# Performance work log

Hardware: AMD Instinct MI355X
Metric: run time of the kernel (lower is better)

The kernel has to match this reference:

```python
import jax, jax.numpy as jnp
import numpy as np

B = 64            # batch of graphs
E = 8978          # edge-simplices per graph (nodes of the Hodge-1 graph)
E2 = E // 2       # after Graclus pair-pooling
K = 4             # Laguerre polynomial order
DEG = 16          # avg degree of the (edge-)adjacency
SLOPE = 0.33      # LeakyReLU negative slope
EPS = 1e-5        # BatchNorm eps


def _make_edges(rng, b, n, deg):
    # block-diagonal batched edge list: each graph only connects within itself
    offs = np.repeat(np.arange(b, dtype=np.int64) * n, n * deg)
    dst = np.tile(np.repeat(np.arange(n, dtype=np.int64), deg), b) + offs
    src = rng.integers(0, n, size=b * n * deg) + offs
    return np.stack([src, dst]).astype(np.int32)


def setup_inputs() -> dict:
    rng = np.random.default_rng(0)
    ks = jax.random.split(jax.random.key(0), 12)
    N1 = B * E
    ei1 = _make_edges(rng, B, E, DEG)
    ei2 = _make_edges(rng, B, E2, DEG)
    return {
        "x_s": jax.random.normal(ks[0], (N1, 1), jnp.float32),
        "edge_index_s": jnp.asarray(ei1),
        "edge_weight_s": jax.random.uniform(ks[1], (ei1.shape[1],), jnp.float32) * (2.0 / DEG),
        "edge_index_s1": jnp.asarray(ei2),
        "edge_weight_s1": jax.random.uniform(ks[2], (ei2.shape[1],), jnp.float32) * (2.0 / DEG),
        "W0": jax.random.normal(ks[3], (K, 1, 32), jnp.float32) * 0.3,
        "b0": jnp.zeros((32,), jnp.float32),
        "g0": jnp.ones((32,), jnp.float32),
        "be0": jnp.zeros((32,), jnp.float32),
        "W1": jax.random.normal(ks[4], (K, 32, 32), jnp.float32) * 0.1,
        "b1": jnp.zeros((32,), jnp.float32),
        "g1": jnp.ones((32,), jnp.float32),
        "be1": jnp.zeros((32,), jnp.float32),
        "W2": jax.random.normal(ks[5], (K, 32, 1), jnp.float32) * 0.1,
        "b2": jnp.zeros((1,), jnp.float32),
        "g2": jnp.ones((1,), jnp.float32),
        "be2": jnp.zeros((1,), jnp.float32),
        "lin1_W": jax.random.normal(ks[6], (E2, 256), jnp.float32) * 0.02,
        "lin1_b": jnp.zeros((256,), jnp.float32),
        "bn1_g": jnp.ones((256,), jnp.float32),
        "bn1_b": jnp.zeros((256,), jnp.float32),
        "lin2_W": jax.random.normal(ks[7], (256, 128), jnp.float32) * 0.06,
        "lin2_b": jnp.zeros((128,), jnp.float32),
        "bn2_g": jnp.ones((128,), jnp.float32),
        "bn2_b": jnp.zeros((128,), jnp.float32),
        "lin3_W": jax.random.normal(ks[8], (128, 1), jnp.float32) * 0.09,
        "lin3_b": jnp.zeros((1,), jnp.float32),
    }


def _laguerre_layer(x, src, dst, ew, W, b, gamma, beta, n):
    """HodgeLaguerreConv (K-order Laguerre recurrence over sparse L) + BatchNorm + LeakyReLU."""
    def matvec(v):  # (L v)[i] = sum_j w_ij v[j]
        return jax.ops.segment_sum(ew[:, None] * v[src], dst, num_segments=n)
    Tp = x                      # L_0(L) x = x
    out = Tp @ W[0]
    Tc = x - matvec(x)          # L_1(L) x = x - L x
    out = out + Tc @ W[1]
    for k in range(1, K - 1):   # L_{k+1} = ((2k+1-L) L_k - k L_{k-1}) / (k+1)
        Tn = ((2 * k + 1) * Tc - matvec(Tc) - k * Tp) / (k + 1)
        out = out + Tn @ W[k + 1]
        Tp, Tc = Tc, Tn
    out = out + b
    out = gamma * (out - out.mean(0)) * jax.lax.rsqrt(out.var(0) + EPS) + beta
    return jnp.where(out > 0, out, SLOPE * out)


def _bn(h, g, b):
    return g * (h - h.mean(0)) * jax.lax.rsqrt(h.var(0) + EPS) + b


def reference(x_s, edge_index_s, edge_weight_s, edge_index_s1, edge_weight_s1,
              W0, b0, g0, be0, W1, b1, g1, be1, W2, b2, g2, be2,
              lin1_W, lin1_b, bn1_g, bn1_b, lin2_W, lin2_b, bn2_g, bn2_b,
              lin3_W, lin3_b):
    N1, N2 = B * E, B * E2
    x = _laguerre_layer(x_s, edge_index_s[0], edge_index_s[1], edge_weight_s,
                        W0, b0, g0, be0, N1)
    # Graclus pooling: merge matched node pairs by max over features
    x = x.reshape(B, E2, 2, x.shape[-1]).max(axis=2).reshape(N2, -1)
    x = _laguerre_layer(x, edge_index_s1[0], edge_index_s1[1], edge_weight_s1,
                        W1, b1, g1, be1, N2)
    x = _laguerre_layer(x, edge_index_s1[0], edge_index_s1[1], edge_weight_s1,
                        W2, b2, g2, be2, N2)
    x = x.reshape(B, E2)        # last conv has 1 channel
    h = jax.nn.relu(_bn(x @ lin1_W + lin1_b, bn1_g, bn1_b))
    h = jax.nn.relu(_bn(h @ lin2_W + lin2_b, bn2_g, bn2_b))
    return h @ lin3_W + lin3_b  # [B, num_classes=1]
```

## Files before the change

### kernel.cpp

```cpp
#include <hip/hip_runtime.h>
#include <cstdint>

#define SLOPE 0.33f

static constexpr int B_   = 64;
static constexpr int E1_  = 8978;
static constexpr int E2_  = 4489;
static constexpr int N1_  = B_ * E1_;
static constexpr int N2_  = B_ * E2_;
static constexpr int DEG_ = 16;
static constexpr int QTR_ = 2245;
static constexpr int QTR2_ = 1123;
static constexpr int MVGRID = (N2_ * 32) / 256;
static constexpr double EPS_ = 1e-5;

typedef unsigned short u16;
typedef unsigned int   u32;

__device__ __forceinline__ float lrelu(float v) { return v > 0.f ? v : SLOPE * v; }
__device__ __forceinline__ float dot4(float4 a, float4 b) {
  return a.x * b.x + a.y * b.y + a.z * b.z + a.w * b.w;
}
__device__ __forceinline__ void gacc(float4& acc, float wgt, const float4& gv) {
  acc.x += wgt * gv.x; acc.y += wgt * gv.y; acc.z += wgt * gv.z; acc.w += wgt * gv.w;
}

template<int NPG>
__global__ __launch_bounds__(256) void k_prep(const int* __restrict__ src, int nNodes,
    u16* __restrict__ out) {
  int node = blockIdx.x * 256 + threadIdx.x;
  if (node >= nNodes) return;
  int gbase = (node / NPG) * NPG;
  const int4* s4 = (const int4*)(src + (size_t)node * DEG_);
  int4 a = s4[0], b = s4[1], c = s4[2], d = s4[3];
  uint4 o0, o1;
  o0.x = (u32)(a.x - gbase) | ((u32)(a.y - gbase) << 16);
  o0.y = (u32)(a.z - gbase) | ((u32)(a.w - gbase) << 16);
  o0.z = (u32)(b.x - gbase) | ((u32)(b.y - gbase) << 16);
  o0.w = (u32)(b.z - gbase) | ((u32)(b.w - gbase) << 16);
  o1.x = (u32)(c.x - gbase) | ((u32)(c.y - gbase) << 16);
  o1.y = (u32)(c.z - gbase) | ((u32)(c.w - gbase) << 16);
  o1.z = (u32)(d.x - gbase) | ((u32)(d.y - gbase) << 16);
  o1.w = (u32)(d.z - gbase) | ((u32)(d.w - gbase) << 16);
  uint4* op = (uint4*)(out + (size_t)node * DEG_);
  op[0] = o0; op[1] = o1;
}

#define GATHER1(dst, sv, si_, w4_)                                              \
  {                                                                             \
    uint4 A_ = si_[0], Bq_ = si_[1];                                            \
    float4 w_;                                                                  \
    w_ = w4_[0];                                                                \
    dst += w_.x * sv[A_.x & 0xFFFFu] + w_.y * sv[A_.x >> 16]                    \
         + w_.z * sv[A_.y & 0xFFFFu] + w_.w * sv[A_.y >> 16];                   \
    w_ = w4_[1];                                                                \
    dst += w_.x * sv[A_.z & 0xFFFFu] + w_.y * sv[A_.z >> 16]                    \
         + w_.z * sv[A_.w & 0xFFFFu] + w_.w * sv[A_.w >> 16];                   \
    w_ = w4_[2];                                                                \
    dst += w_.x * sv[Bq_.x & 0xFFFFu] + w_.y * sv[Bq_.x >> 16]                  \
         + w_.z * sv[Bq_.y & 0xFFFFu] + w_.w * sv[Bq_.y >> 16];                 \
    w_ = w4_[3];                                                                \
    dst += w_.x * sv[Bq_.z & 0xFFFFu] + w_.y * sv[Bq_.z >> 16]                  \
         + w_.z * sv[Bq_.w & 0xFFFFu] + w_.w * sv[Bq_.w >> 16];                 \
  }

__global__ __launch_bounds__(1024) void k0_mv1(const float* __restrict__ x,
    const u16* __restrict__ lsrc, const float* __restrict__ ew, float* __restrict__ T1) {
  __shared__ float sx[E1_];
  int g = blockIdx.x >> 2, q = blockIdx.x & 3;
  int gbase = g * E1_;
  for (int j = threadIdx.x; j < E1_; j += 1024) sx[j] = x[gbase + j];
  __syncthreads();
  int start = q * QTR_, end = min(start + QTR_, E1_);
  for (int i = start + (int)threadIdx.x; i < end; i += 1024) {
    int node = gbase + i;
    const uint4* si = (const uint4*)(lsrc + (size_t)node * DEG_);
    const float4* w4 = (const float4*)(ew + (size_t)node * DEG_);
    float acc = 0.f;
    GATHER1(acc, sx, si, w4);
    T1[node] = sx[i] - acc;
  }
}

__global__ __launch_bounds__(1024) void k0_mv2(const float* __restrict__ x,
    const u16* __restrict__ lsrc, const float* __restrict__ ew,
    const float* __restrict__ T1, float* __restrict__ T2) {
  __shared__ float sT[E1_];
  int g = blockIdx.x >> 2, q = blockIdx.x & 3;
  int gbase = g * E1_;
  for (int j = threadIdx.x; j < E1_; j += 1024) sT[j] = T1[gbase + j];
  __syncthreads();
  int start = q * QTR_, end = min(start + QTR_, E1_);
  for (int i = start + (int)threadIdx.x; i < end; i += 1024) {
    int node = gbase + i;
    const uint4* si = (const uint4*)(lsrc + (size_t)node * DEG_);
    const float4* w4 = (const float4*)(ew + (size_t)node * DEG_);
    float acc = 0.f;
    GATHER1(acc, sT, si, w4);
    T2[node] = (3.f * sT[i] - acc - x[node]) * 0.5f;
  }
}

__global__ __launch_bounds__(1024) void k0_mv3(const float* __restrict__ x,
    const u16* __restrict__ lsrc, const float* __restrict__ ew,
    const float* __restrict__ T1, const float* __restrict__ T2,
    float* __restrict__ T3, double* mom) {
  __shared__ float sT[E1_];
  __shared__ double sred[16 * 14];
  int g = blockIdx.x >> 2, q = blockIdx.x & 3;
  int gbase = g * E1_;
  for (int j = threadIdx.x; j < E1_; j += 1024) sT[j] = T2[gbase + j];
  __syncthreads();
  double m[14];
#pragma unroll
  for (int j = 0; j < 14; ++j) m[j] = 0.0;
  int start = q * QTR_, end = min(start + QTR_, E1_);
  for (int i = start + (int)threadIdx.x; i < end; i += 1024) {
    int node = gbase + i;
    const uint4* si = (const uint4*)(lsrc + (size_t)node * DEG_);
    const float4* w4 = (const float4*)(ew + (size_t)node * DEG_);
    float acc = 0.f;
    GATHER1(acc, sT, si, w4);
    float t1 = T1[node];
    float t2 = sT[i];
    float t3 = (5.f * t2 - acc - 2.f * t1) * (1.f / 3.f);
    T3[node] = t3;
    double d0 = x[node], d1 = t1, d2 = t2, d3 = t3;
    m[0] += d0; m[1] += d1; m[2] += d2; m[3] += d3;
    m[4] += d0 * d0; m[5] += d0 * d1; m[6] += d0 * d2; m[7] += d0 * d3;
    m[8] += d1 * d1; m[9] += d1 * d2; m[10] += d1 * d3;
    m[11] += d2 * d2; m[12] += d2 * d3; m[13] += d3 * d3;
  }
  int lane = threadIdx.x & 63, wid = threadIdx.x >> 6;
#pragma unroll
  for (int j = 0; j < 14; ++j) {
    double v = m[j];
    for (int o = 32; o; o >>= 1) v += __shfl_down(v, o);
    if (lane == 0) sred[wid * 14 + j] = v;
  }
  __syncthreads();
  if (threadIdx.x < 14) {
    double s = 0.0;
#pragma unroll
    for (int w = 0; w < 16; ++w) s += sred[w * 14 + threadIdx.x];
    atomicAdd(&mom[threadIdx.x], s);
  }
}

__global__ void k0_params(const double* __restrict__ mom, const float* __restrict__ W0,
    const float* __restrict__ g0, const float* __restrict__ be0,
    float* __restrict__ scale0, float* __restrict__ shiftE0) {
  int c = threadIdx.x;
  if (c >= 32) return;
  double inv = 1.0 / (double)N1_;
  double mm[4];
#pragma unroll
  for (int k = 0; k < 4; ++k) mm[k] = mom[k] * inv;
  double M[4][4];
  M[0][0] = mom[4] * inv;  M[0][1] = mom[5] * inv;  M[0][2] = mom[6] * inv;  M[0][3] = mom[7] * inv;
  M[1][1] = mom[8] * inv;  M[1][2] = mom[9] * inv;  M[1][3] = mom[10] * inv;
  M[2][2] = mom[11] * inv; M[2][3] = mom[12] * inv; M[3][3] = mom[13] * inv;
  M[1][0] = M[0][1]; M[2][0] = M[0][2]; M[3][0] = M[0][3];
  M[2][1] = M[1][2]; M[3][1] = M[1][3]; M[3][2] = M[2][3];
  double w[4];
#pragma unroll
  for (int k = 0; k < 4; ++k) w[k] = W0[k * 32 + c];
  double mean = 0.0;
#pragma unroll
  for (int k = 0; k < 4; ++k) mean += w[k] * mm[k];
  double e2 = 0.0;
#pragma unroll
  for (int k = 0; k < 4; ++k)
#pragma unroll
    for (int l = 0; l < 4; ++l) e2 += M[k][l] * w[k] * w[l];
  double var = e2 - mean * mean;
  double sc = (double)g0[c] / sqrt(var + EPS_);
  scale0[c] = (float)sc;
  shiftE0[c] = (float)((double)be0[c] - sc * mean);
}

__global__ __launch_bounds__(256) void k0_pool(const float* __restrict__ x,
    const float* __restrict__ T1, const float* __restrict__ T2, const float* __restrict__ T3,
    const float* __restrict__ W0, const float* __restrict__ scale0,
    const float* __restrict__ shiftE0, float* __restrict__ x1) {
  int gid = blockIdx.x * 256 + threadIdx.x;
  int grp = gid >> 5, c = gid & 31;
  if (grp >= N2_) return;
  int b = grp / E2_, j = grp - b * E2_;
  int ga = b * E1_ + 2 * j, gb = ga + 1;
  float w0 = W0[c], w1 = W0[32 + c], w2 = W0[64 + c], w3 = W0[96 + c];
  float da = x[ga] * w0 + T1[ga] * w1 + T2[ga] * w2 + T3[ga] * w3;
  float db = x[gb] * w0 + T1[gb] * w1 + T2[gb] * w2 + T3[gb] * w3;
  float sc = scale0[c], sh = shiftE0[c];
  float ya = lrelu(sc * da + sh), yb = lrelu(sc * db + sh);
  x1[grp * 32 + c] = fmaxf(ya, yb);
}

__global__ __launch_bounds__(256) void k1_prepw(const float* __restrict__ W1,
    float* __restrict__ qb) {
  int idx = blockIdx.x * 256 + threadIdx.x;
  if (idx >= 4096) return;
  int e = idx & 3, rr = (idx >> 2) & 3, qq = (idx >> 4) & 7, oq = idx >> 7;
  int j = oq >> 3, c = (oq & 7) * 4 + rr, in = 4 * qq + e;
  float k0, k1, k2, k3;
  if (j == 0)      { k0 = 0.f; k1 = 0.f; k2 = 0.f;  k3 = -1.f / 6.f; }
  else if (j == 1) { k0 = 0.f; k1 = 0.f; k2 = 0.5f; k3 = 1.5f; }
  else if (j == 2) { k0 = 0.f; k1 = -1.f; k2 = -2.f; k3 = -3.f; }
  else             { k0 = 1.f; k1 = 1.f; k2 = 1.f;  k3 = 1.f; }
  const float* wp = W1 + in * 32 + c;
  qb[idx] = k0 * wp[0] + k1 * wp[1024] + k2 * wp[2048] + k3 * wp[3072];
}

__global__ __launch_bounds__(256) void k1_projall(const float* __restrict__ X,
    const float* __restrict__ qb, float4* __restrict__ P4) {
  int r = blockIdx.x * 256 + threadIdx.x;
  if (r >= N2_) return;
  float4 xr[8];
  const float4* pa = (const float4*)(X + (size_t)r * 32);
#pragma unroll
  for (int t = 0; t < 8; ++t) xr[t] = pa[t];
  const float4* qb4 = (const float4*)qb;
  for (int oq = 0; oq < 32; ++oq) {
    float4 acc = {0.f, 0.f, 0.f, 0.f};
#pragma unroll
    for (int qq = 0; qq < 8; ++qq) {
      const float4* wq = qb4 + (oq * 8 + qq) * 4;
      float4 w0 = wq[0], w1 = wq[1], w2 = wq[2], w3 = wq[3];
      float4 xq = xr[qq];
      acc.x += dot4(xq, w0);
      acc.y += dot4(xq, w1);
      acc.z += dot4(xq, w2);
      acc.w += dot4(xq, w3);
    }
    P4[(size_t)oq * N2_ + r] = acc;
  }
}

__global__ __launch_bounds__(1024) void k1_chain(const float4* __restrict__ P4,
    float4* __restrict__ O4, const u16* __restrict__ lsrc,
    const float* __restrict__ ew, double* st) {
  __shared__ float4 bA[E2_], bB[E2_];
  __shared__ float sacc[8];
  int v = (blockIdx.x & 7) * 64 + (blockIdx.x >> 3);
  int g = v >> 3, cg = v & 7;
  int gbase = g * E2_;
  int tid = threadIdx.x;
  if (tid < 8) sacc[tid] = 0.f;
  {
    const float4* sp = P4 + (size_t)cg * N2_ + gbase;
    for (int i = tid; i < E2_; i += 1024) bA[i] = sp[i];
  }
  float4* cur = bA;
  float4* nxt = bB;
  for (int s = 1; s <= 3; ++s) {
    __syncthreads();
    const float4* selfp = P4 + (size_t)(s * 8 + cg) * N2_ + gbase;
    for (int n = tid; n < E2_; n += 1024) {
      const uint4* si = (const uint4*)(lsrc + (size_t)(gbase + n) * DEG_);
      const float4* w4 = (const float4*)(ew + (size_t)(gbase + n) * DEG_);
      uint4 A = si[0], Bq = si[1];
      float4 acc = selfp[n];
      float4 w;
      w = w4[0];
      gacc(acc, w.x, cur[A.x & 0xFFFFu]); gacc(acc, w.y, cur[A.x >> 16]);
      gacc(acc, w.z, cur[A.y & 0xFFFFu]); gacc(acc, w.w, cur[A.y >> 16]);
      w = w4[1];
      gacc(acc, w.x, cur[A.z & 0xFFFFu]); gacc(acc, w.y, cur[A.z >> 16]);
      gacc(acc, w.z, cur[A.w & 0xFFFFu]); gacc(acc, w.w, cur[A.w >> 16]);
      w = w4[2];
      gacc(acc, w.x, cur[Bq.x & 0xFFFFu]); gacc(acc, w.y, cur[Bq.x >> 16]);
      gacc(acc, w.z, cur[Bq.y & 0xFFFFu]); gacc(acc, w.w, cur[Bq.y >> 16]);
      w = w4[3];
      gacc(acc, w.x, cur[Bq.z & 0xFFFFu]); gacc(acc, w.y, cur[Bq.z >> 16]);
      gacc(acc, w.z, cur[Bq.w & 0xFFFFu]); gacc(acc, w.w, cur[Bq.w >> 16]);
      nxt[n] = acc;
    }
    float4* t = cur; cur = nxt; nxt = t;
  }
  __syncthreads();
  float4* op = O4 + (size_t)cg * N2_ + gbase;
  float4 s1 = {0.f, 0.f, 0.f, 0.f}, s2 = {0.f, 0.f, 0.f, 0.f};
  for (int n = tid; n < E2_; n += 1024) {
    float4 vv = cur[n];
    op[n] = vv;
    s1.x += vv.x; s1.y += vv.y; s1.z += vv.z; s1.w += vv.w;
    s2.x += vv.x * vv.x; s2.y += vv.y * vv.y; s2.z += vv.z * vv.z; s2.w += vv.w * vv.w;
  }
  for (int o = 32; o; o >>= 1) {
    s1.x += __shfl_down(s1.x, o); s1.y += __shfl_down(s1.y, o);
    s1.z += __shfl_down(s1.z, o); s1.w += __shfl_down(s1.w, o);
    s2.x += __shfl_down(s2.x, o); s2.y += __shfl_down(s2.y, o);
    s2.z += __shfl_down(s2.z, o); s2.w += __shfl_down(s2.w, o);
  }
  if ((tid & 63) == 0) {
    atomicAdd(&sacc[0], s1.x); atomicAdd(&sacc[1], s1.y);
    atomicAdd(&sacc[2], s1.z); atomicAdd(&sacc[3], s1.w);
    atomicAdd(&sacc[4], s2.x); atomicAdd(&sacc[5], s2.y);
    atomicAdd(&sacc[6], s2.z); atomicAdd(&sacc[7], s2.w);
  }
  __syncthreads();
  if (tid < 4) {
    int ch = cg * 4 + tid;
    atomicAdd(&st[ch], (double)sacc[tid]);
    atomicAdd(&st[32 + ch], (double)sacc[4 + tid]);
  }
}

__global__ void k1_params(const double* __restrict__ sum, const double* __restrict__ sq,
    const float* __restrict__ g1, const float* __restrict__ be1,
    float* __restrict__ scale1, float* __restrict__ shiftE1) {
  int c = threadIdx.x;
  if (c >= 32) return;
  double mean = sum[c] / (double)N2_;
  double var = sq[c] / (double)N2_ - mean * mean;
  double sc = (double)g1[c] / sqrt(var + EPS_);
  scale1[c] = (float)sc;
  shiftE1[c] = (float)((double)be1[c] - sc * mean);
}

__global__ __launch_bounds__(256) void k2_proj(const float* __restrict__ X,
    const float* __restrict__ W2, const float* __restrict__ scale1,
    const float* __restrict__ shiftE1,
    float* __restrict__ u0, float* __restrict__ u1,
    float* __restrict__ u2, float* __restrict__ u3) {
  __shared__ float qv[4][32];
  __shared__ float fsc[32], fsh[32];
  int tid = threadIdx.x;
  if (tid < 128) {
    int cp = tid & 31, j = tid >> 5;
    float w0 = W2[cp], w1 = W2[32 + cp], w2 = W2[64 + cp], w3 = W2[96 + cp];
    float q;
    if (j == 0)      q = w0 + w1 + w2 + w3;
    else if (j == 1) q = -w1 - 2.f * w2 - 3.f * w3;
    else if (j == 2) q = 0.5f * w2 + 1.5f * w3;
    else             q = -w3 * (1.f / 6.f);
    qv[j][cp] = q;
  }
  if (tid < 32) { fsc[tid] = scale1[tid]; fsh[tid] = shiftE1[tid]; }
  __syncthreads();
  int node = blockIdx.x * 256 + tid;
  if (node >= N2_) return;
  const float4* xf = (const float4*)X;
  float a0 = 0.f, a1 = 0.f, a2 = 0.f, a3 = 0.f;
#pragma unroll
  for (int t = 0; t < 8; ++t) {
    float4 v = xf[(size_t)t * N2_ + node];
    float f0 = lrelu(fsc[4 * t] * v.x + fsh[4 * t]);
    float f1 = lrelu(fsc[4 * t + 1] * v.y + fsh[4 * t + 1]);
    float f2_ = lrelu(fsc[4 * t + 2] * v.z + fsh[4 * t + 2]);
    float f3 = lrelu(fsc[4 * t + 3] * v.w + fsh[4 * t + 3]);
    a0 += f0 * qv[0][4 * t] + f1 * qv[0][4 * t + 1] + f2_ * qv[0][4 * t + 2] + f3 * qv[0][4 * t + 3];
    a1 += f0 * qv[1][4 * t] + f1 * qv[1][4 * t + 1] + f2_ * qv[1][4 * t + 2] + f3 * qv[1][4 * t + 3];
    a2 += f0 * qv[2][4 * t] + f1 * qv[2][4 * t + 1] + f2_ * qv[2][4 * t + 2] + f3 * qv[2][4 * t + 3];
    a3 += f0 * qv[3][4 * t] + f1 * qv[3][4 * t + 1] + f2_ * qv[3][4 * t + 2] + f3 * qv[3][4 * t + 3];
  }
  u0[node] = a0; u1[node] = a1; u2[node] = a2; u3[node] = a3;
}

__global__ __launch_bounds__(1024) void k2_step(const float* __restrict__ z,
    const u16* __restrict__ lsrc, const float* __restrict__ ew,
    const float* __restrict__ u, float* __restrict__ zo,
    int do_stats, double* st2) {
  __shared__ float sz[E2_];
  __shared__ double sred[16][2];
  int g = blockIdx.x >> 2, q = blockIdx.x & 3;
  int gbase = g * E2_;
  for (int j = threadIdx.x; j < E2_; j += 1024) sz[j] = z[gbase + j];
  __syncthreads();
  int start = q * QTR2_, end = min(start + QTR2_, E2_);
  double aS = 0.0, aQ = 0.0;
  for (int i = start + (int)threadIdx.x; i < end; i += 1024) {
    int node = gbase + i;
    const uint4* si = (const uint4*)(lsrc + (size_t)node * DEG_);
    const float4* w4 = (const float4*)(ew + (size_t)node * DEG_);
    float acc = 0.f;
    GATHER1(acc, sz, si, w4);
    float val = u[node] + acc;
    zo[node] = val;
    if (do_stats) { aS += val; aQ += (double)val * (double)val; }
  }
  if (do_stats) {
    int lane = threadIdx.x & 63, wid = threadIdx.x >> 6;
    for (int o = 32; o; o >>= 1) { aS += __shfl_down(aS, o); aQ += __shfl_down(aQ, o); }
    if (lane == 0) { sred[wid][0] = aS; sred[wid][1] = aQ; }
    __syncthreads();
    if (threadIdx.x == 0) {
      double s = 0.0, qq = 0.0;
#pragma unroll
      for (int w = 0; w < 16; ++w) { s += sred[w][0]; qq += sred[w][1]; }
      atomicAdd(&st2[0], s); atomicAdd(&st2[1], qq);
    }
  }
}

__global__ void k2_params(const double* __restrict__ st2, const float* __restrict__ g2,
    const float* __restrict__ be2, float* __restrict__ p ) {
  if (threadIdx.x != 0) return;
  double mean = st2[0] / (double)N2_;
  double var = st2[1] / (double)N2_ - mean * mean;
  double sc = (double)g2[0] / sqrt(var + EPS_);
  p[128] = (float)sc;
  p[129] = (float)((double)be2[0] - sc * mean);
}

__global__ __launch_bounds__(256) void k3_gemm1(const float* __restrict__ out2,
    const float* __restrict__ lin1W, const float* __restrict__ p, float* h1pre) {
  __shared__ float f2v[8][144];
  float sc = p[128], sh = p[129];
  int bs = blockIdx.x & 7, rs = blockIdx.x >> 3;
  int b0 = bs * 8;
  int r0 = rs * 141;
  int nr = min(141, E2_ - r0);
  int c = threadIdx.x;
#pragma unroll
  for (int b = 0; b < 8; ++b)
    for (int j = c; j < 144; j += 256)
      f2v[b][j] = (j < nr) ? lrelu(sc * out2[(b0 + b) * E2_ + r0 + j] + sh) : 0.f;
  __syncthreads();
  float acc[8];
#pragma unroll
  for (int b = 0; b < 8; ++b) acc[b] = 0.f;
  int nr4 = nr & ~3;
  int j = 0;
  for (; j < nr4; j += 4) {
    const float* wp = lin1W + (size_t)(r0 + j) * 256 + c;
    float w0 = wp[0], w1 = wp[256], w2 = wp[512], w3 = wp[768];
#pragma unroll
    for (int b = 0; b < 8; ++b) {
      float4 f = *(const float4*)&f2v[b][j];
      acc[b] += f.x * w0 + f.y * w1 + f.z * w2 + f.w * w3;
    }
  }
  for (; j < nr; ++j) {
    float w = lin1W[(size_t)(r0 + j) * 256 + c];
#pragma unroll
    for (int b = 0; b < 8; ++b) acc[b] += f2v[b][j] * w;
  }
#pragma unroll
  for (int b = 0; b < 8; ++b)
    atomicAdd(&h1pre[(b0 + b) * 256 + c], acc[b]);
}

__global__ __launch_bounds__(256) void k4_bn1(const float* __restrict__ h1pre,
    const float* __restrict__ g, const float* __restrict__ be, float* __restrict__ h1) {
  int c = threadIdx.x;
  float vs[64];
  double s = 0.0, q = 0.0;
  for (int b = 0; b < 64; ++b) { float v = h1pre[b * 256 + c]; vs[b] = v; s += v; q += (double)v * v; }
  double mean = s / 64.0, var = q / 64.0 - mean * mean;
  double scd = (double)g[c] / sqrt(var + EPS_);
  double shd = (double)be[c] - scd * mean;
  for (int b = 0; b < 64; ++b) {
    float y = (float)(scd * vs[b] + shd);
    h1[b * 256 + c] = y > 0.f ? y : 0.f;
  }
}

__global__ __launch_bounds__(256) void k5_gemm2(const float* __restrict__ h1,
    const float* __restrict__ lin2W, float* __restrict__ h2pre) {
  __shared__ float sred[256];
  int c = blockIdx.x;
  int b = threadIdx.x & 63, q = threadIdx.x >> 6;
  float acc = 0.f;
  for (int r = q; r < 256; r += 4) acc += h1[b * 256 + r] * lin2W[r * 128 + c];
  sred[threadIdx.x] = acc;
  __syncthreads();
  if (threadIdx.x < 64)
    h2pre[threadIdx.x * 128 + c] = sred[threadIdx.x] + sred[64 + threadIdx.x]
                                 + sred[128 + threadIdx.x] + sred[192 + threadIdx.x];
}

__global__ __launch_bounds__(256) void k6_final(const float* __restrict__ h2pre,
    const float* __restrict__ g, const float* __restrict__ be,
    const float* __restrict__ W3, const float* __restrict__ b3, float* __restrict__ outp) {
  __shared__ float sh2[64 * 129];
  __shared__ float sred[256];
  int tid = threadIdx.x;
  if (tid < 128) {
    int c = tid;
    float vs[64];
    double s = 0.0, q = 0.0;
    for (int b = 0; b < 64; ++b) { float v = h2pre[b * 128 + c]; vs[b] = v; s += v; q += (double)v * v; }
    double mean = s / 64.0, var = q / 64.0 - mean * mean;
    double scd = (double)g[c] / sqrt(var + EPS_);
    double shd = (double)be[c] - scd * mean;
    for (int b = 0; b < 64; ++b) {
      float y = (float)(scd * vs[b] + shd);
      sh2[b * 129 + c] = y > 0.f ? y : 0.f;
    }
  }
  __syncthreads();
  int b = tid & 63, q = tid >> 6;
  float acc = 0.f;
  for (int r = q; r < 128; r += 4) acc += sh2[b * 129 + r] * W3[r];
  sred[tid] = acc;
  __syncthreads();
  if (tid < 64)
    outp[tid] = sred[tid] + sred[64 + tid] + sred[128 + tid] + sred[192 + tid] + b3[0];
}

extern "C" void kernel_launch(void* const* d_in, const int* in_sizes, int n_in,
                              void* d_out, int out_size, void* d_ws, size_t ws_size,
                              hipStream_t stream) {
  const float* x    = (const float*)d_in[0];
  const int*   ei1  = (const int*)d_in[1];
  const float* ew1  = (const float*)d_in[2];
  const int*   ei2  = (const int*)d_in[3];
  const float* ew2  = (const float*)d_in[4];
  const float* W0   = (const float*)d_in[5];
  const float* g0   = (const float*)d_in[7];
  const float* be0  = (const float*)d_in[8];
  const float* W1   = (const float*)d_in[9];
  const float* g1   = (const float*)d_in[11];
  const float* be1  = (const float*)d_in[12];
  const float* W2   = (const float*)d_in[13];
  const float* g2   = (const float*)d_in[15];
  const float* be2  = (const float*)d_in[16];
  const float* lin1W = (const float*)d_in[17];
  const float* bn1g = (const float*)d_in[19];
  const float* bn1b = (const float*)d_in[20];
  const float* lin2W = (const float*)d_in[21];
  const float* bn2g = (const float*)d_in[23];
  const float* bn2b = (const float*)d_in[24];
  const float* lin3W = (const float*)d_in[25];
  const float* lin3b = (const float*)d_in[26];

  char* ws = (char*)d_ws;
  double* stats  = (double*)ws;
  float*  params = (float*)(ws + 1024);
  float*  h1pre  = (float*)(ws + 4096);
  float*  h1     = (float*)(ws + 4096 + 65536);
  float*  h2pre  = (float*)(ws + 4096 + 131072);
  float*  qb     = (float*)(ws + 196608);
  float*  Treg   = (float*)(ws + 262144);
  float* T1_0 = Treg;
  float* T2_0 = Treg + N1_;
  float* T3_0 = Treg + 2 * (size_t)N1_;
  float* u0   = Treg;
  float* u1   = Treg + (size_t)N2_;
  float* u2   = Treg + 2 * (size_t)N2_;
  float* u3   = Treg + 3 * (size_t)N2_;
  float* zA   = Treg + 4 * (size_t)N2_;
  float* out2 = Treg + 5 * (size_t)N2_;
  float*  big = (float*)(ws + 262144 + 3 * (size_t)N1_ * 4);
  float* bufA = big;
  float* Pbuf = big + 32 * (size_t)N2_;
  u16* lsrc1 = (u16*)Pbuf;
  u16* lsrc2 = (u16*)bufA;

  hipMemsetAsync(stats, 0, 80 * sizeof(double), stream);
  hipMemsetAsync(h1pre, 0, 65536, stream);

  k_prep<E1_><<<(N1_ + 255) / 256, 256, 0, stream>>>(ei1, N1_, lsrc1);
  k1_prepw<<<16, 256, 0, stream>>>(W1, qb);

  k0_mv1<<<256, 1024, 0, stream>>>(x, lsrc1, ew1, T1_0);
  k0_mv2<<<256, 1024, 0, stream>>>(x, lsrc1, ew1, T1_0, T2_0);
  k0_mv3<<<256, 1024, 0, stream>>>(x, lsrc1, ew1, T1_0, T2_0, T3_0, stats);
  k0_params<<<1, 32, 0, stream>>>(stats, W0, g0, be0, params, params + 32);
  k0_pool<<<MVGRID, 256, 0, stream>>>(x, T1_0, T2_0, T3_0, W0, params, params + 32, bufA);

  k1_projall<<<(N2_ + 255) / 256, 256, 0, stream>>>(bufA, qb, (float4*)Pbuf);
  k_prep<E2_><<<(N2_ + 255) / 256, 256, 0, stream>>>(ei2, N2_, lsrc2);
  k1_chain<<<512, 1024, 0, stream>>>((const float4*)Pbuf, (float4*)Pbuf, lsrc2, ew2, stats + 14);
  k1_params<<<1, 32, 0, stream>>>(stats + 14, stats + 46, g1, be1, params + 64, params + 96);

  k2_proj<<<(N2_ + 255) / 256, 256, 0, stream>>>(Pbuf, W2, params + 64, params + 96,
                                                 u0, u1, u2, u3);
  k2_step<<<256, 1024, 0, stream>>>(u3, lsrc2, ew2, u2, zA, 0, nullptr);
  k2_step<<<256, 1024, 0, stream>>>(zA, lsrc2, ew2, u1, u3, 0, nullptr);
  k2_step<<<256, 1024, 0, stream>>>(u3, lsrc2, ew2, u0, out2, 1, stats + 78);
  k2_params<<<1, 64, 0, stream>>>(stats + 78, g2, be2, params);

  k3_gemm1<<<256, 256, 0, stream>>>(out2, lin1W, params, h1pre);
  k4_bn1<<<1, 256, 0, stream>>>(h1pre, bn1g, bn1b, h1);
  k5_gemm2<<<128, 256, 0, stream>>>(h1, lin2W, h2pre);
  k6_final<<<1, 256, 0, stream>>>(h2pre, bn2g, bn2b, lin3W, lin3b, (float*)d_out);
}
```

Measured before the change: 496.6 us.

## Fuse prep kernels, pool with projection, BN1 into GEMM2; resplit SpMV grids

Three preprocessing kernels (edge index compaction for both graphs and weight prep) are merged into one launch. Graclus pooling is fused with the layer-1 projection, so the 32-channel pooled tensor is never written to or read back from memory, and BN0's scale is folded into W0. BN1 with ReLU is fused into the second GEMM, with each block recomputing the batch statistics redundantly. The SpMV step kernels go from 256 blocks of 1024 threads to 512 blocks of 512, which improves occupancy and load balance but stages each graph's vector in shared memory twice as often.

```diff
diff --git a/kernel.cpp b/kernel.cpp
--- a/kernel.cpp
+++ b/kernel.cpp
@@ -9,9 +9,8 @@
 static constexpr int N1_  = B_ * E1_;
 static constexpr int N2_  = B_ * E2_;
 static constexpr int DEG_ = 16;
-static constexpr int QTR_ = 2245;
-static constexpr int QTR2_ = 1123;
-static constexpr int MVGRID = (N2_ * 32) / 256;
+static constexpr int SLC1_ = 1123;
+static constexpr int SLC2_ = 562;
 static constexpr double EPS_ = 1e-5;
 
 typedef unsigned short u16;
@@ -26,10 +25,8 @@
 }
 
 template<int NPG>
-__global__ __launch_bounds__(256) void k_prep(const int* __restrict__ src, int nNodes,
+__device__ __forceinline__ void comp_idx(const int* __restrict__ src, int node,
     u16* __restrict__ out) {
-  int node = blockIdx.x * 256 + threadIdx.x;
-  if (node >= nNodes) return;
   int gbase = (node / NPG) * NPG;
   const int4* s4 = (const int4*)(src + (size_t)node * DEG_);
   int4 a = s4[0], b = s4[1], c = s4[2], d = s4[3];
@@ -44,6 +41,32 @@
   o1.w = (u32)(d.z - gbase) | ((u32)(d.w - gbase) << 16);
   uint4* op = (uint4*)(out + (size_t)node * DEG_);
   op[0] = o0; op[1] = o1;
+}
+
+__global__ __launch_bounds__(256) void k_prep_all(const int* __restrict__ src1,
+    const int* __restrict__ src2, const float* __restrict__ W1,
+    u16* __restrict__ lsrc1, u16* __restrict__ lsrc2, float* __restrict__ qb) {
+  int blk = blockIdx.x;
+  if (blk < 2245) {
+    int node = blk * 256 + threadIdx.x;
+    if (node < N1_) comp_idx<E1_>(src1, node, lsrc1);
+  } else if (blk < 3368) {
+    int node = (blk - 2245) * 256 + threadIdx.x;
+    if (node < N2_) comp_idx<E2_>(src2, node, lsrc2);
+  } else {
+    int idx = (blk - 3368) * 256 + threadIdx.x;
+    if (idx < 4096) {
+      int e = idx & 3, rr = (idx >> 2) & 3, qq = (idx >> 4) & 7, oq = idx >> 7;
+      int j = oq >> 3, c = (oq & 7) * 4 + rr, in = 4 * qq + e;
+      float k0, k1, k2, k3;
+      if (j == 0)      { k0 = 0.f; k1 = 0.f; k2 = 0.f;  k3 = -1.f / 6.f; }
+      else if (j == 1) { k0 = 0.f; k1 = 0.f; k2 = 0.5f; k3 = 1.5f; }
+      else if (j == 2) { k0 = 0.f; k1 = -1.f; k2 = -2.f; k3 = -3.f; }
+      else             { k0 = 1.f; k1 = 1.f; k2 = 1.f;  k3 = 1.f; }
+      const float* wp = W1 + in * 32 + c;
+      qb[idx] = k0 * wp[0] + k1 * wp[1024] + k2 * wp[2048] + k3 * wp[3072];
+    }
+  }
 }
 
 #define GATHER1(dst, sv, si_, w4_)                                              \
@@ -64,15 +87,15 @@
          + w_.z * sv[Bq_.w & 0xFFFFu] + w_.w * sv[Bq_.w >> 16];                 \
   }
 
-__global__ __launch_bounds__(1024) void k0_mv1(const float* __restrict__ x,
+__global__ __launch_bounds__(512) void k0_mv1(const float* __restrict__ x,
     const u16* __restrict__ lsrc, const float* __restrict__ ew, float* __restrict__ T1) {
   __shared__ float sx[E1_];
-  int g = blockIdx.x >> 2, q = blockIdx.x & 3;
+  int g = blockIdx.x >> 3, q = blockIdx.x & 7;
   int gbase = g * E1_;
-  for (int j = threadIdx.x; j < E1_; j += 1024) sx[j] = x[gbase + j];
-  __syncthreads();
-  int start = q * QTR_, end = min(start + QTR_, E1_);
-  for (int i = start + (int)threadIdx.x; i < end; i += 1024) {
+  for (int j = threadIdx.x; j < E1_; j += 512) sx[j] = x[gbase + j];
+  __syncthreads();
+  int start = q * SLC1_, end = min(start + SLC1_, E1_);
+  for (int i = start + (int)threadIdx.x; i < end; i += 512) {
     int node = gbase + i;
     const uint4* si = (const uint4*)(lsrc + (size_t)node * DEG_);
     const float4* w4 = (const float4*)(ew + (size_t)node * DEG_);
@@ -82,16 +105,16 @@
   }
 }
 
-__global__ __launch_bounds__(1024) void k0_mv2(const float* __restrict__ x,
+__global__ __launch_bounds__(512) void k0_mv2(const float* __restrict__ x,
     const u16* __restrict__ lsrc, const float* __restrict__ ew,
     const float* __restrict__ T1, float* __restrict__ T2) {
   __shared__ float sT[E1_];
-  int g = blockIdx.x >> 2, q = blockIdx.x & 3;
+  int g = blockIdx.x >> 3, q = blockIdx.x & 7;
   int gbase = g * E1_;
-  for (int j = threadIdx.x; j < E1_; j += 1024) sT[j] = T1[gbase + j];
-  __syncthreads();
-  int start = q * QTR_, end = min(start + QTR_, E1_);
-  for (int i = start + (int)threadIdx.x; i < end; i += 1024) {
+  for (int j = threadIdx.x; j < E1_; j += 512) sT[j] = T1[gbase + j];
+  __syncthreads();
+  int start = q * SLC1_, end = min(start + SLC1_, E1_);
+  for (int i = start + (int)threadIdx.x; i < end; i += 512) {
     int node = gbase + i;
     const uint4* si = (const uint4*)(lsrc + (size_t)node * DEG_);
     const float4* w4 = (const float4*)(ew + (size_t)node * DEG_);
@@ -101,21 +124,21 @@
   }
 }
 
-__global__ __launch_bounds__(1024) void k0_mv3(const float* __restrict__ x,
+__global__ __launch_bounds__(512) void k0_mv3(const float* __restrict__ x,
     const u16* __restrict__ lsrc, const float* __restrict__ ew,
     const float* __restrict__ T1, const float* __restrict__ T2,
     float* __restrict__ T3, double* mom) {
   __shared__ float sT[E1_];
-  __shared__ double sred[16 * 14];
-  int g = blockIdx.x >> 2, q = blockIdx.x & 3;
+  __shared__ double sred[8 * 14];
+  int g = blockIdx.x >> 3, q = blockIdx.x & 7;
   int gbase = g * E1_;
-  for (int j = threadIdx.x; j < E1_; j += 1024) sT[j] = T2[gbase + j];
+  for (int j = threadIdx.x; j < E1_; j += 512) sT[j] = T2[gbase + j];
   __syncthreads();
   double m[14];
 #pragma unroll
   for (int j = 0; j < 14; ++j) m[j] = 0.0;
-  int start = q * QTR_, end = min(start + QTR_, E1_);
-  for (int i = start + (int)threadIdx.x; i < end; i += 1024) {
+  int start = q * SLC1_, end = min(start + SLC1_, E1_);
+  for (int i = start + (int)threadIdx.x; i < end; i += 512) {
     int node = gbase + i;
     const uint4* si = (const uint4*)(lsrc + (size_t)node * DEG_);
     const float4* w4 = (const float4*)(ew + (size_t)node * DEG_);
@@ -142,14 +165,14 @@
   if (threadIdx.x < 14) {
     double s = 0.0;
 #pragma unroll
-    for (int w = 0; w < 16; ++w) s += sred[w * 14 + threadIdx.x];
+    for (int w = 0; w < 8; ++w) s += sred[w * 14 + threadIdx.x];
     atomicAdd(&mom[threadIdx.x], s);
   }
 }
 
 __global__ void k0_params(const double* __restrict__ mom, const float* __restrict__ W0,
     const float* __restrict__ g0, const float* __restrict__ be0,
-    float* __restrict__ scale0, float* __restrict__ shiftE0) {
+    float* __restrict__ scale0, float* __restrict__ shiftE0, float* __restrict__ scW0) {
   int c = threadIdx.x;
   if (c >= 32) return;
   double inv = 1.0 / (double)N1_;
@@ -177,62 +200,82 @@
   double sc = (double)g0[c] / sqrt(var + EPS_);
   scale0[c] = (float)sc;
   shiftE0[c] = (float)((double)be0[c] - sc * mean);
-}
-
-__global__ __launch_bounds__(256) void k0_pool(const float* __restrict__ x,
+#pragma unroll
+  for (int k = 0; k < 4; ++k) scW0[c * 4 + k] = (float)(sc * w[k]);
+}
+
+__global__ __launch_bounds__(256) void k_poolproj(const float* __restrict__ x,
     const float* __restrict__ T1, const float* __restrict__ T2, const float* __restrict__ T3,
-    const float* __restrict__ W0, const float* __restrict__ scale0,
-    const float* __restrict__ shiftE0, float* __restrict__ x1) {
-  int gid = blockIdx.x * 256 + threadIdx.x;
-  int grp = gid >> 5, c = gid & 31;
-  if (grp >= N2_) return;
-  int b = grp / E2_, j = grp - b * E2_;
-  int ga = b * E1_ + 2 * j, gb = ga + 1;
-  float w0 = W0[c], w1 = W0[32 + c], w2 = W0[64 + c], w3 = W0[96 + c];
-  float da = x[ga] * w0 + T1[ga] * w1 + T2[ga] * w2 + T3[ga] * w3;
-  float db = x[gb] * w0 + T1[gb] * w1 + T2[gb] * w2 + T3[gb] * w3;
-  float sc = scale0[c], sh = shiftE0[c];
-  float ya = lrelu(sc * da + sh), yb = lrelu(sc * db + sh);
-  x1[grp * 32 + c] = fmaxf(ya, yb);
-}
-
-__global__ __launch_bounds__(256) void k1_prepw(const float* __restrict__ W1,
-    float* __restrict__ qb) {
-  int idx = blockIdx.x * 256 + threadIdx.x;
-  if (idx >= 4096) return;
-  int e = idx & 3, rr = (idx >> 2) & 3, qq = (idx >> 4) & 7, oq = idx >> 7;
-  int j = oq >> 3, c = (oq & 7) * 4 + rr, in = 4 * qq + e;
-  float k0, k1, k2, k3;
-  if (j == 0)      { k0 = 0.f; k1 = 0.f; k2 = 0.f;  k3 = -1.f / 6.f; }
-  else if (j == 1) { k0 = 0.f; k1 = 0.f; k2 = 0.5f; k3 = 1.5f; }
-  else if (j == 2) { k0 = 0.f; k1 = -1.f; k2 = -2.f; k3 = -3.f; }
-  else             { k0 = 1.f; k1 = 1.f; k2 = 1.f;  k3 = 1.f; }
-  const float* wp = W1 + in * 32 + c;
-  qb[idx] = k0 * wp[0] + k1 * wp[1024] + k2 * wp[2048] + k3 * wp[3072];
-}
-
-__global__ __launch_bounds__(256) void k1_projall(const float* __restrict__ X,
+    const float* __restrict__ scW0, const float* __restrict__ shiftE0,
     const float* __restrict__ qb, float4* __restrict__ P4) {
-  int r = blockIdx.x * 256 + threadIdx.x;
-  if (r >= N2_) return;
-  float4 xr[8];
-  const float4* pa = (const float4*)(X + (size_t)r * 32);
-#pragma unroll
-  for (int t = 0; t < 8; ++t) xr[t] = pa[t];
+  int rA = blockIdx.x * 512 + threadIdx.x;
+  int rB = rA + 256;
+  bool okA = rA < N2_, okB = rB < N2_;
+  if (!okA) return;
+  const float4* wt = (const float4*)scW0;
+  float4 xA[8], xB[8];
+  {
+    int b = rA / E2_, j = rA - b * E2_;
+    int ga = b * E1_ + 2 * j;
+    float2 xv = *(const float2*)(x + ga);
+    float2 t1 = *(const float2*)(T1 + ga);
+    float2 t2 = *(const float2*)(T2 + ga);
+    float2 t3 = *(const float2*)(T3 + ga);
+#pragma unroll
+    for (int c8 = 0; c8 < 8; ++c8) {
+      float4 o;
+#pragma unroll
+      for (int e = 0; e < 4; ++e) {
+        int c = c8 * 4 + e;
+        float4 w = wt[c];
+        float sh = shiftE0[c];
+        float da = w.x * xv.x + w.y * t1.x + w.z * t2.x + w.w * t3.x + sh;
+        float db = w.x * xv.y + w.y * t1.y + w.z * t2.y + w.w * t3.y + sh;
+        float v = fmaxf(lrelu(da), lrelu(db));
+        if (e == 0) o.x = v; else if (e == 1) o.y = v; else if (e == 2) o.z = v; else o.w = v;
+      }
+      xA[c8] = o;
+    }
+  }
+  if (okB) {
+    int b = rB / E2_, j = rB - b * E2_;
+    int ga = b * E1_ + 2 * j;
+    float2 xv = *(const float2*)(x + ga);
+    float2 t1 = *(const float2*)(T1 + ga);
+    float2 t2 = *(const float2*)(T2 + ga);
+    float2 t3 = *(const float2*)(T3 + ga);
+#pragma unroll
+    for (int c8 = 0; c8 < 8; ++c8) {
+      float4 o;
+#pragma unroll
+      for (int e = 0; e < 4; ++e) {
+        int c = c8 * 4 + e;
+        float4 w = wt[c];
+        float sh = shiftE0[c];
+        float da = w.x * xv.x + w.y * t1.x + w.z * t2.x + w.w * t3.x + sh;
+        float db = w.x * xv.y + w.y * t1.y + w.z * t2.y + w.w * t3.y + sh;
+        float v = fmaxf(lrelu(da), lrelu(db));
+        if (e == 0) o.x = v; else if (e == 1) o.y = v; else if (e == 2) o.z = v; else o.w = v;
+      }
+      xB[c8] = o;
+    }
+  } else {
+#pragma unroll
+    for (int t = 0; t < 8; ++t) xB[t] = {0.f, 0.f, 0.f, 0.f};
+  }
   const float4* qb4 = (const float4*)qb;
   for (int oq = 0; oq < 32; ++oq) {
-    float4 acc = {0.f, 0.f, 0.f, 0.f};
+    float4 aA = {0.f, 0.f, 0.f, 0.f}, aB = {0.f, 0.f, 0.f, 0.f};
 #pragma unroll
     for (int qq = 0; qq < 8; ++qq) {
       const float4* wq = qb4 + (oq * 8 + qq) * 4;
       float4 w0 = wq[0], w1 = wq[1], w2 = wq[2], w3 = wq[3];
-      float4 xq = xr[qq];
-      acc.x += dot4(xq, w0);
-      acc.y += dot4(xq, w1);
-      acc.z += dot4(xq, w2);
-      acc.w += dot4(xq, w3);
-    }
-    P4[(size_t)oq * N2_ + r] = acc;
+      float4 xa = xA[qq], xb = xB[qq];
+      aA.x += dot4(xa, w0); aA.y += dot4(xa, w1); aA.z += dot4(xa, w2); aA.w += dot4(xa, w3);
+      aB.x += dot4(xb, w0); aB.y += dot4(xb, w1); aB.z += dot4(xb, w2); aB.w += dot4(xb, w3);
+    }
+    P4[(size_t)oq * N2_ + rA] = aA;
+    if (okB) P4[(size_t)oq * N2_ + rB] = aB;
   }
 }
 
@@ -357,19 +400,19 @@
   u0[node] = a0; u1[node] = a1; u2[node] = a2; u3[node] = a3;
 }
 
-__global__ __launch_bounds__(1024) void k2_step(const float* __restrict__ z,
+__global__ __launch_bounds__(512) void k2_step(const float* __restrict__ z,
     const u16* __restrict__ lsrc, const float* __restrict__ ew,
     const float* __restrict__ u, float* __restrict__ zo,
     int do_stats, double* st2) {
   __shared__ float sz[E2_];
-  __shared__ double sred[16][2];
-  int g = blockIdx.x >> 2, q = blockIdx.x & 3;
+  __shared__ double sred[8][2];
+  int g = blockIdx.x >> 3, q = blockIdx.x & 7;
   int gbase = g * E2_;
-  for (int j = threadIdx.x; j < E2_; j += 1024) sz[j] = z[gbase + j];
-  __syncthreads();
-  int start = q * QTR2_, end = min(start + QTR2_, E2_);
+  for (int j = threadIdx.x; j < E2_; j += 512) sz[j] = z[gbase + j];
+  __syncthreads();
+  int start = q * SLC2_, end = min(start + SLC2_, E2_);
   double aS = 0.0, aQ = 0.0;
-  for (int i = start + (int)threadIdx.x; i < end; i += 1024) {
+  for (int i = start + (int)threadIdx.x; i < end; i += 512) {
     int node = gbase + i;
     const uint4* si = (const uint4*)(lsrc + (size_t)node * DEG_);
     const float4* w4 = (const float4*)(ew + (size_t)node * DEG_);
@@ -387,7 +430,7 @@
     if (threadIdx.x == 0) {
       double s = 0.0, qq = 0.0;
 #pragma unroll
-      for (int w = 0; w < 16; ++w) { s += sred[w][0]; qq += sred[w][1]; }
+      for (int w = 0; w < 8; ++w) { s += sred[w][0]; qq += sred[w][1]; }
       atomicAdd(&st2[0], s); atomicAdd(&st2[1], qq);
     }
   }
@@ -441,33 +484,41 @@
     atomicAdd(&h1pre[(b0 + b) * 256 + c], acc[b]);
 }
 
-__global__ __launch_bounds__(256) void k4_bn1(const float* __restrict__ h1pre,
-    const float* __restrict__ g, const float* __restrict__ be, float* __restrict__ h1) {
-  int c = threadIdx.x;
-  float vs[64];
-  double s = 0.0, q = 0.0;
-  for (int b = 0; b < 64; ++b) { float v = h1pre[b * 256 + c]; vs[b] = v; s += v; q += (double)v * v; }
-  double mean = s / 64.0, var = q / 64.0 - mean * mean;
-  double scd = (double)g[c] / sqrt(var + EPS_);
-  double shd = (double)be[c] - scd * mean;
-  for (int b = 0; b < 64; ++b) {
-    float y = (float)(scd * vs[b] + shd);
-    h1[b * 256 + c] = y > 0.f ? y : 0.f;
-  }
-}
-
-__global__ __launch_bounds__(256) void k5_gemm2(const float* __restrict__ h1,
+__global__ __launch_bounds__(256) void k5_gemm2bn(const float* __restrict__ h1pre,
+    const float* __restrict__ g, const float* __restrict__ be,
     const float* __restrict__ lin2W, float* __restrict__ h2pre) {
+  __shared__ float sh1[64 * 257];
   __shared__ float sred[256];
   int c = blockIdx.x;
-  int b = threadIdx.x & 63, q = threadIdx.x >> 6;
+  int tid = threadIdx.x;
+  for (int i = tid; i < 64 * 256; i += 256) {
+    int b = i >> 8, cc = i & 255;
+    sh1[b * 257 + cc] = h1pre[i];
+  }
+  __syncthreads();
+  {
+    int cc = tid;
+    double s = 0.0, qd = 0.0;
+    float vs[64];
+#pragma unroll
+    for (int b = 0; b < 64; ++b) { float v = sh1[b * 257 + cc]; vs[b] = v; s += v; qd += (double)v * v; }
+    double mean = s / 64.0, var = qd / 64.0 - mean * mean;
+    double scd = (double)g[cc] / sqrt(var + EPS_);
+    double shd = (double)be[cc] - scd * mean;
+#pragma unroll
+    for (int b = 0; b < 64; ++b) {
+      float y = (float)(scd * vs[b] + shd);
+      sh1[b * 257 + cc] = y > 0.f ? y : 0.f;
+    }
+  }
+  __syncthreads();
+  int b = tid & 63, q = tid >> 6;
   float acc = 0.f;
-  for (int r = q; r < 256; r += 4) acc += h1[b * 256 + r] * lin2W[r * 128 + c];
-  sred[threadIdx.x] = acc;
-  __syncthreads();
-  if (threadIdx.x < 64)
-    h2pre[threadIdx.x * 128 + c] = sred[threadIdx.x] + sred[64 + threadIdx.x]
-                                 + sred[128 + threadIdx.x] + sred[192 + threadIdx.x];
+  for (int r = q; r < 256; r += 4) acc += sh1[b * 257 + r] * lin2W[r * 128 + c];
+  sred[tid] = acc;
+  __syncthreads();
+  if (tid < 64)
+    h2pre[tid * 128 + c] = sred[tid] + sred[64 + tid] + sred[128 + tid] + sred[192 + tid];
 }
 
 __global__ __launch_bounds__(256) void k6_final(const float* __restrict__ h2pre,
@@ -529,7 +580,6 @@
   double* stats  = (double*)ws;
   float*  params = (float*)(ws + 1024);
   float*  h1pre  = (float*)(ws + 4096);
-  float*  h1     = (float*)(ws + 4096 + 65536);
   float*  h2pre  = (float*)(ws + 4096 + 131072);
   float*  qb     = (float*)(ws + 196608);
   float*  Treg   = (float*)(ws + 262144);
@@ -551,29 +601,27 @@
   hipMemsetAsync(stats, 0, 80 * sizeof(double), stream);
   hipMemsetAsync(h1pre, 0, 65536, stream);
 
-  k_prep<E1_><<<(N1_ + 255) / 256, 256, 0, stream>>>(ei1, N1_, lsrc1);
-  k1_prepw<<<16, 256, 0, stream>>>(W1, qb);
-
-  k0_mv1<<<256, 1024, 0, stream>>>(x, lsrc1, ew1, T1_0);
-  k0_mv2<<<256, 1024, 0, stream>>>(x, lsrc1, ew1, T1_0, T2_0);
-  k0_mv3<<<256, 1024, 0, stream>>>(x, lsrc1, ew1, T1_0, T2_0, T3_0, stats);
-  k0_params<<<1, 32, 0, stream>>>(stats, W0, g0, be0, params, params + 32);
-  k0_pool<<<MVGRID, 256, 0, stream>>>(x, T1_0, T2_0, T3_0, W0, params, params + 32, bufA);
-
-  k1_projall<<<(N2_ + 255) / 256, 256, 0, stream>>>(bufA, qb, (float4*)Pbuf);
-  k_prep<E2_><<<(N2_ + 255) / 256, 256, 0, stream>>>(ei2, N2_, lsrc2);
+  k_prep_all<<<3384, 256, 0, stream>>>(ei1, ei2, W1, lsrc1, lsrc2, qb);
+
+  k0_mv1<<<512, 512, 0, stream>>>(x, lsrc1, ew1, T1_0);
+  k0_mv2<<<512, 512, 0, stream>>>(x, lsrc1, ew1, T1_0, T2_0);
+  k0_mv3<<<512, 512, 0, stream>>>(x, lsrc1, ew1, T1_0, T2_0, T3_0, stats);
+  k0_params<<<1, 32, 0, stream>>>(stats, W0, g0, be0, params, params + 32, params + 160);
+
+  k_poolproj<<<(N2_ + 511) / 512, 256, 0, stream>>>(x, T1_0, T2_0, T3_0,
+                                                    params + 160, params + 32, qb, (float4*)Pbuf);
+
   k1_chain<<<512, 1024, 0, stream>>>((const float4*)Pbuf, (float4*)Pbuf, lsrc2, ew2, stats + 14);
   k1_params<<<1, 32, 0, stream>>>(stats + 14, stats + 46, g1, be1, params + 64, params + 96);
 
   k2_proj<<<(N2_ + 255) / 256, 256, 0, stream>>>(Pbuf, W2, params + 64, params + 96,
                                                  u0, u1, u2, u3);
-  k2_step<<<256, 1024, 0, stream>>>(u3, lsrc2, ew2, u2, zA, 0, nullptr);
-  k2_step<<<256, 1024, 0, stream>>>(zA, lsrc2, ew2, u1, u3, 0, nullptr);
-  k2_step<<<256, 1024, 0, stream>>>(u3, lsrc2, ew2, u0, out2, 1, stats + 78);
+  k2_step<<<512, 512, 0, stream>>>(u3, lsrc2, ew2, u2, zA, 0, nullptr);
+  k2_step<<<512, 512, 0, stream>>>(zA, lsrc2, ew2, u1, u3, 0, nullptr);
+  k2_step<<<512, 512, 0, stream>>>(u3, lsrc2, ew2, u0, out2, 1, stats + 78);
   k2_params<<<1, 64, 0, stream>>>(stats + 78, g2, be2, params);
 
   k3_gemm1<<<256, 256, 0, stream>>>(out2, lin1W, params, h1pre);
-  k4_bn1<<<1, 256, 0, stream>>>(h1pre, bn1g, bn1b, h1);
-  k5_gemm2<<<128, 256, 0, stream>>>(h1, lin2W, h2pre);
+  k5_gemm2bn<<<128, 256, 0, stream>>>(h1pre, bn1g, bn1b, lin2W, h2pre);
   k6_final<<<1, 256, 0, stream>>>(h2pre, bn2g, bn2b, lin3W, lin3b, (float*)d_out);
 }
```

Measured after the change: 610.1 us. 1.23x slower.
